# Kernel tuning notes

Measured on AMD Instinct MI355X. Metric: run time of the kernel, lower is better.

The kernel has to match this reference:

```python
import jax, jax.numpy as jnp
import numpy as np
from jax.scipy.special import gammaln

N_I = 100000
N_J = 100000
D = 8
S_I = 6000
S_J = 6000
NNZ = 500000
EPS = 1e-06


def setup_inputs() -> dict:
    key = jax.random.key(0)
    ks = jax.random.split(key, 9)
    beta = jax.random.normal(ks[0], (N_I,), dtype=jnp.float32)
    gamma = jax.random.normal(ks[1], (N_J,), dtype=jnp.float32)
    latent_zi = jax.random.normal(ks[2], (N_I, D), dtype=jnp.float32)
    latent_zj = jax.random.normal(ks[3], (N_J, D), dtype=jnp.float32)
    # multinomial-without-replacement node samples -> random permutation prefix
    sample_i_idx = jax.random.permutation(ks[4], N_I)[:S_I]
    sample_j_idx = jax.random.permutation(ks[5], N_J)[:S_J]
    # spspmm-selected subgraph links (global node indices) with edge counts
    sparse_i_sample = jax.random.randint(ks[6], (NNZ,), 0, N_I)
    sparse_j_sample = jax.random.randint(ks[7], (NNZ,), 0, N_J)
    valueC = jax.random.uniform(ks[8], (NNZ,), dtype=jnp.float32)
    return {
        'beta': beta, 'gamma': gamma,
        'latent_zi': latent_zi, 'latent_zj': latent_zj,
        'valueC': valueC,
        'sample_i_idx': sample_i_idx, 'sample_j_idx': sample_j_idx,
        'sparse_i_sample': sparse_i_sample, 'sparse_j_sample': sparse_j_sample,
    }


def reference(beta, gamma, latent_zi, latent_zj, valueC,
              sample_i_idx, sample_j_idx, sparse_i_sample, sparse_j_sample):
    # Dense non-link term over sampled (I, J) block
    zi = latent_zi[sample_i_idx]            # [S_I, D]
    zj = latent_zj[sample_j_idx]            # [S_J, D]
    diff = zi[:, None, :] - zj[None, :, :] + EPS   # [S_I, S_J, D]
    z_dist = jnp.sqrt(jnp.sum(diff * diff, axis=-1))  # [S_I, S_J]
    Lambda = beta[sample_i_idx][:, None] + gamma[sample_j_idx][None, :] - z_dist
    # Sparse link terms (Poisson log-likelihood)
    dl = latent_zi[sparse_i_sample] - latent_zj[sparse_j_sample] + EPS  # [NNZ, D]
    z_dist_links = jnp.sqrt(jnp.sum(dl * dl, axis=-1))                  # [NNZ]
    bias_links = beta[sparse_i_sample] + gamma[sparse_j_sample]
    log_Lambda_links = valueC * (bias_links - z_dist_links)
    LL = jnp.sum(log_Lambda_links - gammaln(valueC + 1.0)) - jnp.sum(jnp.exp(Lambda))
    return LL
```

## Files before the change

kernel.cpp:

```cpp
#include <hip/hip_runtime.h>
#include <hip/hip_fp16.h>
#include <math.h>

#define NI_TOT 100000
#define NJ_TOT 100000
#define DD 8
#define SI_N 6000
#define SJ_N 6000
#define NNZ_N 500000
#define EPSF 1e-6f
#define LOG2E 1.44269504088896f

#define TI 64
#define JPT 2
#define JTILE (256 * JPT)
#define ND_I ((SI_N + TI - 1) / TI)
#define NJT ((SJ_N + JTILE - 1) / JTILE)
#define N_DENSE_BLOCKS (ND_I * NJT)
#define LPT 2
#define SPARSE_SPAN (256 * LPT)
#define N_SPARSE_BLOCKS ((NNZ_N + SPARSE_SPAN - 1) / SPARSE_SPAN)
#define N_TOTAL_BLOCKS (N_DENSE_BLOCKS + N_SPARSE_BLOCKS)

#define NROWS (NI_TOT + NJ_TOT)
#define HZ_BYTES ((size_t)NROWS * DD * 2)
#define HB_BYTES ((size_t)NROWS * 2)
#define PARTIALS_OFF (HZ_BYTES + HB_BYTES)

#define GA1 (-0.577191652f)
#define GA2 ( 0.988205891f)
#define GA3 (-0.897056937f)
#define GA4 ( 0.918206857f)
#define GA5 (-0.756704078f)
#define GA6 ( 0.482199394f)
#define GA7 (-0.193527818f)
#define GA8 ( 0.035868343f)

__global__ __launch_bounds__(256) void pack_kernel(
    const float* __restrict__ beta, const float* __restrict__ gamma,
    const float* __restrict__ zi_all, const float* __restrict__ zj_all,
    __half* __restrict__ hz, __half* __restrict__ hb)
{
    const int r = blockIdx.x * 256 + threadIdx.x;
    if (r < NROWS) {
        const float* src = (r < NI_TOT) ? zi_all + (size_t)r * DD
                                        : zj_all + (size_t)(r - NI_TOT) * DD;
        float4 a = ((const float4*)src)[0];
        float4 b = ((const float4*)src)[1];
        __half2 h0 = __floats2half2_rn(a.x, a.y);
        __half2 h1 = __floats2half2_rn(a.z, a.w);
        __half2 h2 = __floats2half2_rn(b.x, b.y);
        __half2 h3 = __floats2half2_rn(b.z, b.w);
        uint4 u;
        u.x = *(unsigned*)&h0; u.y = *(unsigned*)&h1;
        u.z = *(unsigned*)&h2; u.w = *(unsigned*)&h3;
        ((uint4*)hz)[r] = u;
    } else if (r < 2 * NROWS) {
        const int q = r - NROWS;
        float v = (q < NI_TOT) ? beta[q] : gamma[q - NI_TOT];
        hb[q] = __float2half(v);
    }
}

__device__ __forceinline__ void unpack_row(uint4 u, float f[DD]) {
    float2 p;
    p = __half22float2(*(__half2*)&u.x); f[0] = p.x; f[1] = p.y;
    p = __half22float2(*(__half2*)&u.y); f[2] = p.x; f[3] = p.y;
    p = __half22float2(*(__half2*)&u.z); f[4] = p.x; f[5] = p.y;
    p = __half22float2(*(__half2*)&u.w); f[6] = p.x; f[7] = p.y;
}

__global__ __launch_bounds__(256) void fused_kernel(
    const float* __restrict__ beta, const float* __restrict__ gamma,
    const float* __restrict__ zi_all, const float* __restrict__ zj_all,
    const float* __restrict__ valueC,
    const int* __restrict__ si, const int* __restrict__ sj,
    const int* __restrict__ spi, const int* __restrict__ spj,
    const __half* __restrict__ hz, const __half* __restrict__ hb,
    float* __restrict__ partials, float* __restrict__ out, int mode)
{
    __shared__ float sRed[4];
    const int t = threadIdx.x;

    float blocksum = 0.0f;

    if (blockIdx.x < N_DENSE_BLOCKS) {
        __shared__ __align__(16) float  sZi[TI * DD];
        __shared__ __align__(8)  float2 sIB[TI];

        const int it = blockIdx.x % ND_I;
        const int js = blockIdx.x / ND_I;
        const int i0 = it * TI;

        for (int idx = t; idx < TI * DD; idx += 256) {
            int r = idx >> 3, d = idx & 7;
            int gi = i0 + r;
            float v = (gi < SI_N) ? zi_all[(size_t)si[gi] * DD + d] : 0.0f;
            sZi[idx] = (v + EPSF) * LOG2E;
        }
        __syncthreads();
        if (t < TI) {
            int gi = i0 + t;
            float s = 0.0f;
#pragma unroll
            for (int d = 0; d < DD; ++d) {
                float v = sZi[t * DD + d];
                s = fmaf(v, v, s);
            }
            float bL = (gi < SI_N) ? beta[si[gi]] * LOG2E : -1e30f;
            sIB[t] = make_float2(s, bL);
        }

        const int jb = js * JTILE + t * JPT;
        float zA[DD], zB[DD], glA, glB, s2A, s2B;
        {
            int gj = jb;
            if (gj < SJ_N) {
                int row = sj[gj];
                const float4* q = (const float4*)(zj_all + (size_t)row * DD);
                float4 q0 = q[0], q1 = q[1];
                zA[0]=q0.x*LOG2E; zA[1]=q0.y*LOG2E; zA[2]=q0.z*LOG2E; zA[3]=q0.w*LOG2E;
                zA[4]=q1.x*LOG2E; zA[5]=q1.y*LOG2E; zA[6]=q1.z*LOG2E; zA[7]=q1.w*LOG2E;
                glA = gamma[row] * LOG2E;
            } else {
#pragma unroll
                for (int d = 0; d < DD; ++d) zA[d] = 0.0f;
                glA = -1e30f;
            }
            gj = jb + 1;
            if (gj < SJ_N) {
                int row = sj[gj];
                const float4* q = (const float4*)(zj_all + (size_t)row * DD);
                float4 q0 = q[0], q1 = q[1];
                zB[0]=q0.x*LOG2E; zB[1]=q0.y*LOG2E; zB[2]=q0.z*LOG2E; zB[3]=q0.w*LOG2E;
                zB[4]=q1.x*LOG2E; zB[5]=q1.y*LOG2E; zB[6]=q1.z*LOG2E; zB[7]=q1.w*LOG2E;
                glB = gamma[row] * LOG2E;
            } else {
#pragma unroll
                for (int d = 0; d < DD; ++d) zB[d] = 0.0f;
                glB = -1e30f;
            }
            float sa = 0.0f, sb = 0.0f;
#pragma unroll
            for (int d = 0; d < DD; ++d) {
                sa = fmaf(zA[d], zA[d], sa);
                sb = fmaf(zB[d], zB[d], sb);
            }
            s2A = sa; s2B = sb;
        }
        __syncthreads();

        float acc0 = 0.0f, acc1 = 0.0f;
        float4 cr0 = *(const float4*)&sZi[0];
        float4 cr1 = *(const float4*)&sZi[4];
        float2 cib = sIB[0];
#pragma unroll 4
        for (int a = 0; a < TI; ++a) {
            float4 nr0, nr1; float2 nib;
            if (a + 1 < TI) {
                nr0 = *(const float4*)&sZi[(a + 1) * DD];
                nr1 = *(const float4*)&sZi[(a + 1) * DD + 4];
                nib = sIB[a + 1];
            }
            float dA = 0.0f, dB = 0.0f;
            dA = fmaf(cr0.x, zA[0], dA); dB = fmaf(cr0.x, zB[0], dB);
            dA = fmaf(cr0.y, zA[1], dA); dB = fmaf(cr0.y, zB[1], dB);
            dA = fmaf(cr0.z, zA[2], dA); dB = fmaf(cr0.z, zB[2], dB);
            dA = fmaf(cr0.w, zA[3], dA); dB = fmaf(cr0.w, zB[3], dB);
            dA = fmaf(cr1.x, zA[4], dA); dB = fmaf(cr1.x, zB[4], dB);
            dA = fmaf(cr1.y, zA[5], dA); dB = fmaf(cr1.y, zB[5], dB);
            dA = fmaf(cr1.z, zA[6], dA); dB = fmaf(cr1.z, zB[6], dB);
            dA = fmaf(cr1.w, zA[7], dA); dB = fmaf(cr1.w, zB[7], dB);
            float ssA = fmaf(dA, -2.0f, cib.x + s2A);
            float ssB = fmaf(dB, -2.0f, cib.x + s2B);
            ssA = fmaxf(ssA, 1e-20f);
            ssB = fmaxf(ssB, 1e-20f);
            float xA = cib.y + glA - __builtin_amdgcn_sqrtf(ssA);
            float xB = cib.y + glB - __builtin_amdgcn_sqrtf(ssB);
            acc0 += __builtin_amdgcn_exp2f(xA);
            acc1 += __builtin_amdgcn_exp2f(xB);
            cr0 = nr0; cr1 = nr1; cib = nib;
        }
        blocksum = -(acc0 + acc1);
    } else {
        const int base = (blockIdx.x - N_DENSE_BLOCKS) * SPARSE_SPAN + t;
        float val = 0.0f;
        const uint4* hzv = (const uint4*)hz;
#pragma unroll
        for (int u = 0; u < LPT; ++u) {
            const int idx = base + u * 256;
            if (idx >= NNZ_N) continue;
            const int i = spi[idx], j = spj[idx];
            const float c = valueC[idx];
            float dist, bg;
            if (mode == 0) {
                uint4 ui = hzv[i];
                uint4 uj = hzv[NI_TOT + j];
                float fi[DD], fj[DD];
                unpack_row(ui, fi);
                unpack_row(uj, fj);
                float ss = 0.0f;
#pragma unroll
                for (int d = 0; d < DD; ++d) {
                    float df = fi[d] - fj[d] + EPSF;
                    ss = fmaf(df, df, ss);
                }
                ss = fmaxf(ss, 1e-20f);
                dist = __builtin_amdgcn_sqrtf(ss);
                bg = __half2float(hb[i]) + __half2float(hb[NI_TOT + j]);
            } else {
                const float4* zi4 = (const float4*)(zi_all + (size_t)i * DD);
                const float4* zj4 = (const float4*)(zj_all + (size_t)j * DD);
                float4 a0 = zi4[0], a1 = zi4[1];
                float4 b0 = zj4[0], b1 = zj4[1];
                float ss = 0.0f, df;
                df = a0.x-b0.x+EPSF; ss = fmaf(df,df,ss);
                df = a0.y-b0.y+EPSF; ss = fmaf(df,df,ss);
                df = a0.z-b0.z+EPSF; ss = fmaf(df,df,ss);
                df = a0.w-b0.w+EPSF; ss = fmaf(df,df,ss);
                df = a1.x-b1.x+EPSF; ss = fmaf(df,df,ss);
                df = a1.y-b1.y+EPSF; ss = fmaf(df,df,ss);
                df = a1.z-b1.z+EPSF; ss = fmaf(df,df,ss);
                df = a1.w-b1.w+EPSF; ss = fmaf(df,df,ss);
                ss = fmaxf(ss, 1e-20f);
                dist = __builtin_amdgcn_sqrtf(ss);
                bg = beta[i] + gamma[j];
            }
            float g = 1.0f + c*(GA1 + c*(GA2 + c*(GA3 + c*(GA4 + c*(GA5
                          + c*(GA6 + c*(GA7 + c*GA8)))))));
            val += c * (bg - dist) - __builtin_amdgcn_logf(g) * (1.0f / LOG2E);
        }
        blocksum = val;
    }

    float acc = blocksum;
#pragma unroll
    for (int off = 32; off; off >>= 1) acc += __shfl_down(acc, off, 64);
    const int lane = t & 63, w = t >> 6;
    if (lane == 0) sRed[w] = acc;
    __syncthreads();
    if (t == 0) {
        float s = sRed[0] + sRed[1] + sRed[2] + sRed[3];
        if (mode) atomicAdd(out, s);
        else partials[blockIdx.x] = s;
    }
}

__global__ __launch_bounds__(256) void final_reduce_kernel(
    const float* __restrict__ p, int n, float* __restrict__ out)
{
    __shared__ float sRed[4];
    float s0 = 0.0f, s1 = 0.0f, s2 = 0.0f, s3 = 0.0f;
    int i = threadIdx.x;
    for (; i + 768 < n; i += 1024) {
        s0 += p[i]; s1 += p[i + 256]; s2 += p[i + 512]; s3 += p[i + 768];
    }
    for (; i < n; i += 256) s0 += p[i];
    float s = (s0 + s1) + (s2 + s3);
#pragma unroll
    for (int off = 32; off; off >>= 1) s += __shfl_down(s, off, 64);
    const int lane = threadIdx.x & 63, w = threadIdx.x >> 6;
    if (lane == 0) sRed[w] = s;
    __syncthreads();
    if (threadIdx.x == 0) out[0] = sRed[0] + sRed[1] + sRed[2] + sRed[3];
}

extern "C" void kernel_launch(void* const* d_in, const int* in_sizes, int n_in,
                              void* d_out, int out_size, void* d_ws, size_t ws_size,
                              hipStream_t stream) {
    const float* beta   = (const float*)d_in[0];
    const float* gamma  = (const float*)d_in[1];
    const float* zi     = (const float*)d_in[2];
    const float* zj     = (const float*)d_in[3];
    const float* valueC = (const float*)d_in[4];
    const int* si   = (const int*)d_in[5];
    const int* sjx  = (const int*)d_in[6];
    const int* spi  = (const int*)d_in[7];
    const int* spj  = (const int*)d_in[8];
    float* out = (float*)d_out;

    const int ntot = N_TOTAL_BLOCKS;
    const size_t need = PARTIALS_OFF + (size_t)ntot * sizeof(float);

    if (ws_size >= need) {
        __half* hz = (__half*)d_ws;
        __half* hb = (__half*)((char*)d_ws + HZ_BYTES);
        float* p = (float*)((char*)d_ws + PARTIALS_OFF);
        const int packb = (2 * NROWS + 255) / 256;
        pack_kernel<<<packb, 256, 0, stream>>>(beta, gamma, zi, zj, hz, hb);
        fused_kernel<<<ntot, 256, 0, stream>>>(
            beta, gamma, zi, zj, valueC, si, sjx, spi, spj, hz, hb, p, out, 0);
        final_reduce_kernel<<<1, 256, 0, stream>>>(p, ntot, out);
    } else {
        hipMemsetAsync(out, 0, sizeof(float), stream);
        fused_kernel<<<ntot, 256, 0, stream>>>(
            beta, gamma, zi, zj, valueC, si, sjx, spi, spj,
            (const __half*)zi, (const __half*)zi, nullptr, out, 1);
    }
}
```

Before: 109.4 us.

## Factor bias exponentials out of dense loop, drop fp16 pack kernel, widen per-thread tiles

The dense term is rewritten as exp(beta)*exp(gamma)*exp(-dist). The bias exponentials are computed once per row and column, so the inner loop only does an exp2 of the negated distance and an fma. The -2 factor is folded into the staged zi values. The fp16 pack kernel and half-precision sparse gathers are removed, so sparse links read fp32 rows directly and one launch is saved. Work per thread doubles for both the dense tile (JPT 4) and the sparse span (LPT 4), which changes block counts and register pressure and could overflow if exp(beta) is large.

```diff
diff --git a/kernel.cpp b/kernel.cpp
--- a/kernel.cpp
+++ b/kernel.cpp
@@ -1,5 +1,4 @@
 #include <hip/hip_runtime.h>
-#include <hip/hip_fp16.h>
 #include <math.h>
 
 #define NI_TOT 100000
@@ -10,22 +9,18 @@
 #define NNZ_N 500000
 #define EPSF 1e-6f
 #define LOG2E 1.44269504088896f
+#define INV_LOG2E 0.693147180559945f
 
 #define TI 64
-#define JPT 2
+#define JPT 4
 #define JTILE (256 * JPT)
 #define ND_I ((SI_N + TI - 1) / TI)
 #define NJT ((SJ_N + JTILE - 1) / JTILE)
 #define N_DENSE_BLOCKS (ND_I * NJT)
-#define LPT 2
+#define LPT 4
 #define SPARSE_SPAN (256 * LPT)
 #define N_SPARSE_BLOCKS ((NNZ_N + SPARSE_SPAN - 1) / SPARSE_SPAN)
 #define N_TOTAL_BLOCKS (N_DENSE_BLOCKS + N_SPARSE_BLOCKS)
-
-#define NROWS (NI_TOT + NJ_TOT)
-#define HZ_BYTES ((size_t)NROWS * DD * 2)
-#define HB_BYTES ((size_t)NROWS * 2)
-#define PARTIALS_OFF (HZ_BYTES + HB_BYTES)
 
 #define GA1 (-0.577191652f)
 #define GA2 ( 0.988205891f)
@@ -36,58 +31,22 @@
 #define GA7 (-0.193527818f)
 #define GA8 ( 0.035868343f)
 
-__global__ __launch_bounds__(256) void pack_kernel(
-    const float* __restrict__ beta, const float* __restrict__ gamma,
-    const float* __restrict__ zi_all, const float* __restrict__ zj_all,
-    __half* __restrict__ hz, __half* __restrict__ hb)
-{
-    const int r = blockIdx.x * 256 + threadIdx.x;
-    if (r < NROWS) {
-        const float* src = (r < NI_TOT) ? zi_all + (size_t)r * DD
-                                        : zj_all + (size_t)(r - NI_TOT) * DD;
-        float4 a = ((const float4*)src)[0];
-        float4 b = ((const float4*)src)[1];
-        __half2 h0 = __floats2half2_rn(a.x, a.y);
-        __half2 h1 = __floats2half2_rn(a.z, a.w);
-        __half2 h2 = __floats2half2_rn(b.x, b.y);
-        __half2 h3 = __floats2half2_rn(b.z, b.w);
-        uint4 u;
-        u.x = *(unsigned*)&h0; u.y = *(unsigned*)&h1;
-        u.z = *(unsigned*)&h2; u.w = *(unsigned*)&h3;
-        ((uint4*)hz)[r] = u;
-    } else if (r < 2 * NROWS) {
-        const int q = r - NROWS;
-        float v = (q < NI_TOT) ? beta[q] : gamma[q - NI_TOT];
-        hb[q] = __float2half(v);
-    }
-}
-
-__device__ __forceinline__ void unpack_row(uint4 u, float f[DD]) {
-    float2 p;
-    p = __half22float2(*(__half2*)&u.x); f[0] = p.x; f[1] = p.y;
-    p = __half22float2(*(__half2*)&u.y); f[2] = p.x; f[3] = p.y;
-    p = __half22float2(*(__half2*)&u.z); f[4] = p.x; f[5] = p.y;
-    p = __half22float2(*(__half2*)&u.w); f[6] = p.x; f[7] = p.y;
-}
-
 __global__ __launch_bounds__(256) void fused_kernel(
     const float* __restrict__ beta, const float* __restrict__ gamma,
     const float* __restrict__ zi_all, const float* __restrict__ zj_all,
     const float* __restrict__ valueC,
     const int* __restrict__ si, const int* __restrict__ sj,
     const int* __restrict__ spi, const int* __restrict__ spj,
-    const __half* __restrict__ hz, const __half* __restrict__ hb,
     float* __restrict__ partials, float* __restrict__ out, int mode)
 {
     __shared__ float sRed[4];
+    __shared__ __align__(16) float  sZi[TI * DD];
+    __shared__ __align__(8)  float2 sIB[TI];
+
     const int t = threadIdx.x;
-
     float blocksum = 0.0f;
 
     if (blockIdx.x < N_DENSE_BLOCKS) {
-        __shared__ __align__(16) float  sZi[TI * DD];
-        __shared__ __align__(8)  float2 sIB[TI];
-
         const int it = blockIdx.x % ND_I;
         const int js = blockIdx.x / ND_I;
         const int i0 = it * TI;
@@ -96,7 +55,7 @@
             int r = idx >> 3, d = idx & 7;
             int gi = i0 + r;
             float v = (gi < SI_N) ? zi_all[(size_t)si[gi] * DD + d] : 0.0f;
-            sZi[idx] = (v + EPSF) * LOG2E;
+            sZi[idx] = (v + EPSF) * (-2.0f * LOG2E);
         }
         __syncthreads();
         if (t < TI) {
@@ -104,53 +63,39 @@
             float s = 0.0f;
 #pragma unroll
             for (int d = 0; d < DD; ++d) {
-                float v = sZi[t * DD + d];
-                s = fmaf(v, v, s);
-            }
-            float bL = (gi < SI_N) ? beta[si[gi]] * LOG2E : -1e30f;
-            sIB[t] = make_float2(s, bL);
+                float m = sZi[t * DD + d];
+                s = fmaf(m, m, s);
+            }
+            float eb = 0.0f;
+            if (gi < SI_N) eb = __builtin_amdgcn_exp2f(beta[si[gi]] * LOG2E);
+            sIB[t] = make_float2(0.25f * s, eb);
         }
 
         const int jb = js * JTILE + t * JPT;
-        float zA[DD], zB[DD], glA, glB, s2A, s2B;
-        {
-            int gj = jb;
+        float zc[JPT][DD], s2[JPT], gf[JPT];
+#pragma unroll
+        for (int u = 0; u < JPT; ++u) {
+            int gj = jb + u;
             if (gj < SJ_N) {
                 int row = sj[gj];
                 const float4* q = (const float4*)(zj_all + (size_t)row * DD);
                 float4 q0 = q[0], q1 = q[1];
-                zA[0]=q0.x*LOG2E; zA[1]=q0.y*LOG2E; zA[2]=q0.z*LOG2E; zA[3]=q0.w*LOG2E;
-                zA[4]=q1.x*LOG2E; zA[5]=q1.y*LOG2E; zA[6]=q1.z*LOG2E; zA[7]=q1.w*LOG2E;
-                glA = gamma[row] * LOG2E;
+                zc[u][0]=q0.x*LOG2E; zc[u][1]=q0.y*LOG2E; zc[u][2]=q0.z*LOG2E; zc[u][3]=q0.w*LOG2E;
+                zc[u][4]=q1.x*LOG2E; zc[u][5]=q1.y*LOG2E; zc[u][6]=q1.z*LOG2E; zc[u][7]=q1.w*LOG2E;
+                gf[u] = __builtin_amdgcn_exp2f(gamma[row] * LOG2E);
             } else {
 #pragma unroll
-                for (int d = 0; d < DD; ++d) zA[d] = 0.0f;
-                glA = -1e30f;
-            }
-            gj = jb + 1;
-            if (gj < SJ_N) {
-                int row = sj[gj];
-                const float4* q = (const float4*)(zj_all + (size_t)row * DD);
-                float4 q0 = q[0], q1 = q[1];
-                zB[0]=q0.x*LOG2E; zB[1]=q0.y*LOG2E; zB[2]=q0.z*LOG2E; zB[3]=q0.w*LOG2E;
-                zB[4]=q1.x*LOG2E; zB[5]=q1.y*LOG2E; zB[6]=q1.z*LOG2E; zB[7]=q1.w*LOG2E;
-                glB = gamma[row] * LOG2E;
-            } else {
-#pragma unroll
-                for (int d = 0; d < DD; ++d) zB[d] = 0.0f;
-                glB = -1e30f;
-            }
-            float sa = 0.0f, sb = 0.0f;
-#pragma unroll
-            for (int d = 0; d < DD; ++d) {
-                sa = fmaf(zA[d], zA[d], sa);
-                sb = fmaf(zB[d], zB[d], sb);
-            }
-            s2A = sa; s2B = sb;
+                for (int d = 0; d < DD; ++d) zc[u][d] = 0.0f;
+                gf[u] = 0.0f;
+            }
+            float s = 0.0f;
+#pragma unroll
+            for (int d = 0; d < DD; ++d) s = fmaf(zc[u][d], zc[u][d], s);
+            s2[u] = s;
         }
         __syncthreads();
 
-        float acc0 = 0.0f, acc1 = 0.0f;
+        float acc[JPT] = {0.0f, 0.0f, 0.0f, 0.0f};
         float4 cr0 = *(const float4*)&sZi[0];
         float4 cr1 = *(const float4*)&sZi[4];
         float2 cib = sIB[0];
@@ -162,53 +107,37 @@
                 nr1 = *(const float4*)&sZi[(a + 1) * DD + 4];
                 nib = sIB[a + 1];
             }
-            float dA = 0.0f, dB = 0.0f;
-            dA = fmaf(cr0.x, zA[0], dA); dB = fmaf(cr0.x, zB[0], dB);
-            dA = fmaf(cr0.y, zA[1], dA); dB = fmaf(cr0.y, zB[1], dB);
-            dA = fmaf(cr0.z, zA[2], dA); dB = fmaf(cr0.z, zB[2], dB);
-            dA = fmaf(cr0.w, zA[3], dA); dB = fmaf(cr0.w, zB[3], dB);
-            dA = fmaf(cr1.x, zA[4], dA); dB = fmaf(cr1.x, zB[4], dB);
-            dA = fmaf(cr1.y, zA[5], dA); dB = fmaf(cr1.y, zB[5], dB);
-            dA = fmaf(cr1.z, zA[6], dA); dB = fmaf(cr1.z, zB[6], dB);
-            dA = fmaf(cr1.w, zA[7], dA); dB = fmaf(cr1.w, zB[7], dB);
-            float ssA = fmaf(dA, -2.0f, cib.x + s2A);
-            float ssB = fmaf(dB, -2.0f, cib.x + s2B);
-            ssA = fmaxf(ssA, 1e-20f);
-            ssB = fmaxf(ssB, 1e-20f);
-            float xA = cib.y + glA - __builtin_amdgcn_sqrtf(ssA);
-            float xB = cib.y + glB - __builtin_amdgcn_sqrtf(ssB);
-            acc0 += __builtin_amdgcn_exp2f(xA);
-            acc1 += __builtin_amdgcn_exp2f(xB);
+#pragma unroll
+            for (int u = 0; u < JPT; ++u) {
+                float dd;
+                dd = fmaf(cr0.x, zc[u][0], cib.x);
+                dd = fmaf(cr0.y, zc[u][1], dd);
+                dd = fmaf(cr0.z, zc[u][2], dd);
+                dd = fmaf(cr0.w, zc[u][3], dd);
+                dd = fmaf(cr1.x, zc[u][4], dd);
+                dd = fmaf(cr1.y, zc[u][5], dd);
+                dd = fmaf(cr1.z, zc[u][6], dd);
+                dd = fmaf(cr1.w, zc[u][7], dd);
+                float ss = fmaxf(dd + s2[u], 1e-20f);
+                float dist = __builtin_amdgcn_sqrtf(ss);
+                float e = __builtin_amdgcn_exp2f(-dist);
+                acc[u] = fmaf(cib.y, e, acc[u]);
+            }
             cr0 = nr0; cr1 = nr1; cib = nib;
         }
-        blocksum = -(acc0 + acc1);
+        float bs = 0.0f;
+#pragma unroll
+        for (int u = 0; u < JPT; ++u) bs = fmaf(gf[u], acc[u], bs);
+        blocksum = -bs;
     } else {
         const int base = (blockIdx.x - N_DENSE_BLOCKS) * SPARSE_SPAN + t;
         float val = 0.0f;
-        const uint4* hzv = (const uint4*)hz;
 #pragma unroll
         for (int u = 0; u < LPT; ++u) {
             const int idx = base + u * 256;
-            if (idx >= NNZ_N) continue;
-            const int i = spi[idx], j = spj[idx];
-            const float c = valueC[idx];
-            float dist, bg;
-            if (mode == 0) {
-                uint4 ui = hzv[i];
-                uint4 uj = hzv[NI_TOT + j];
-                float fi[DD], fj[DD];
-                unpack_row(ui, fi);
-                unpack_row(uj, fj);
-                float ss = 0.0f;
-#pragma unroll
-                for (int d = 0; d < DD; ++d) {
-                    float df = fi[d] - fj[d] + EPSF;
-                    ss = fmaf(df, df, ss);
-                }
-                ss = fmaxf(ss, 1e-20f);
-                dist = __builtin_amdgcn_sqrtf(ss);
-                bg = __half2float(hb[i]) + __half2float(hb[NI_TOT + j]);
-            } else {
+            if (idx < NNZ_N) {
+                const int i = spi[idx], j = spj[idx];
+                const float c = valueC[idx];
                 const float4* zi4 = (const float4*)(zi_all + (size_t)i * DD);
                 const float4* zj4 = (const float4*)(zj_all + (size_t)j * DD);
                 float4 a0 = zi4[0], a1 = zi4[1];
@@ -223,12 +152,12 @@
                 df = a1.z-b1.z+EPSF; ss = fmaf(df,df,ss);
                 df = a1.w-b1.w+EPSF; ss = fmaf(df,df,ss);
                 ss = fmaxf(ss, 1e-20f);
-                dist = __builtin_amdgcn_sqrtf(ss);
-                bg = beta[i] + gamma[j];
-            }
-            float g = 1.0f + c*(GA1 + c*(GA2 + c*(GA3 + c*(GA4 + c*(GA5
-                          + c*(GA6 + c*(GA7 + c*GA8)))))));
-            val += c * (bg - dist) - __builtin_amdgcn_logf(g) * (1.0f / LOG2E);
+                float dist = __builtin_amdgcn_sqrtf(ss);
+                float bg = beta[i] + gamma[j];
+                float g = 1.0f + c*(GA1 + c*(GA2 + c*(GA3 + c*(GA4 + c*(GA5
+                              + c*(GA6 + c*(GA7 + c*GA8)))))));
+                val += c * (bg - dist) - __builtin_amdgcn_logf(g) * INV_LOG2E;
+            }
         }
         blocksum = val;
     }
@@ -250,13 +179,8 @@
     const float* __restrict__ p, int n, float* __restrict__ out)
 {
     __shared__ float sRed[4];
-    float s0 = 0.0f, s1 = 0.0f, s2 = 0.0f, s3 = 0.0f;
-    int i = threadIdx.x;
-    for (; i + 768 < n; i += 1024) {
-        s0 += p[i]; s1 += p[i + 256]; s2 += p[i + 512]; s3 += p[i + 768];
-    }
-    for (; i < n; i += 256) s0 += p[i];
-    float s = (s0 + s1) + (s2 + s3);
+    float s = 0.0f;
+    for (int i = threadIdx.x; i < n; i += 256) s += p[i];
 #pragma unroll
     for (int off = 32; off; off >>= 1) s += __shfl_down(s, off, 64);
     const int lane = threadIdx.x & 63, w = threadIdx.x >> 6;
@@ -280,21 +204,16 @@
     float* out = (float*)d_out;
 
     const int ntot = N_TOTAL_BLOCKS;
-    const size_t need = PARTIALS_OFF + (size_t)ntot * sizeof(float);
-
-    if (ws_size >= need) {
-        __half* hz = (__half*)d_ws;
-        __half* hb = (__half*)((char*)d_ws + HZ_BYTES);
-        float* p = (float*)((char*)d_ws + PARTIALS_OFF);
-        const int packb = (2 * NROWS + 255) / 256;
-        pack_kernel<<<packb, 256, 0, stream>>>(beta, gamma, zi, zj, hz, hb);
+    const size_t need = (size_t)ntot * sizeof(float);
+
+    if (d_ws && ws_size >= need) {
+        float* p = (float*)d_ws;
         fused_kernel<<<ntot, 256, 0, stream>>>(
-            beta, gamma, zi, zj, valueC, si, sjx, spi, spj, hz, hb, p, out, 0);
+            beta, gamma, zi, zj, valueC, si, sjx, spi, spj, p, out, 0);
         final_reduce_kernel<<<1, 256, 0, stream>>>(p, ntot, out);
     } else {
         hipMemsetAsync(out, 0, sizeof(float), stream);
         fused_kernel<<<ntot, 256, 0, stream>>>(
-            beta, gamma, zi, zj, valueC, si, sjx, spi, spj,
-            (const __half*)zi, (const __half*)zi, nullptr, out, 1);
+            beta, gamma, zi, zj, valueC, si, sjx, spi, spj, nullptr, out, 1);
     }
 }
```

Measured after the change: 113.8 us. 4.0% more time.
